# Performance work log

Hardware: AMD Instinct MI355X
Metric: run time of the kernel (lower is better)

The kernel has to match this reference:

```python
import jax, jax.numpy as jnp
import numpy as np

N1 = 128      # neurons_1
N2 = 128      # neurons_2
K = 8         # num_cluster
G = 1000      # number of graphs
NPG = 500     # nodes per graph
N = G * NPG   # total nodes
NEG_SLOPE = 0.45


def setup_inputs() -> dict:
    key = jax.random.key(0)
    ks = jax.random.split(key, 5)
    x = jax.random.normal(ks[0], (N, N1), dtype=jnp.float32)
    cls = jax.random.randint(ks[1], (N,), 0, K, dtype=jnp.int32)
    batch = jnp.repeat(jnp.arange(G, dtype=jnp.int32), NPG)  # sorted graph ids
    W1 = jax.random.normal(ks[2], (N1, N2), dtype=jnp.float32) * 0.05
    b1 = jnp.zeros((N2,), dtype=jnp.float32)
    Wa = jax.random.normal(ks[3], (N2, 1), dtype=jnp.float32) * 0.05
    ba = jnp.zeros((1,), dtype=jnp.float32)
    return {"x": x, "W1": W1, "b1": b1, "Wa": Wa, "ba": ba, "cls": cls, "batch": batch}


def reference(x, W1, b1, Wa, ba, cls, batch):
    # ---- unpooling_featurizer, cluster_method='fixed' (GI-M2), vectorized ----
    # composite segment id: one segment per (graph, cluster)
    seg = batch.astype(jnp.int32) * K + cls.astype(jnp.int32)          # [N]
    csum = jax.ops.segment_sum(x, seg, num_segments=G * K)             # [G*K, N1]
    counts = jax.ops.segment_sum(jnp.ones((N,), jnp.float32), seg,
                                 num_segments=G * K)                   # [G*K]
    # fixed: random_sets == cls, so gather each node's own cluster sum.
    # ratio_i = counts[cls_i]/Ng, renormalized over graph -> counts[cls_i]/sum_k counts_k^2
    cnode = counts[seg]                                                # [N]
    denom = jax.ops.segment_sum(cnode, batch, num_segments=G)          # [G] = sum_k c_k^2
    ratio = cnode / denom[batch]                                       # [N]
    r_x = csum[seg] * ratio[:, None]                                   # [N, N1]
    # ---- attention MLP ----
    h = jax.nn.leaky_relu(r_x @ W1 + b1, negative_slope=NEG_SLOPE)     # [N, N2]
    logits = (h @ Wa + ba)[:, 0]                                       # [N]
    # ---- segment softmax over graphs ----
    m = jax.ops.segment_max(logits, batch, num_segments=G)             # [G]
    z = jnp.exp(logits - m[batch])
    s = jax.ops.segment_sum(z, batch, num_segments=G)
    return (z / s[batch])[:, None]                                     # [N, 1]
```

## Files before the change

kernel.cpp:

```cpp
#include <hip/hip_runtime.h>

#define GG 1000
#define NPG 500
#define KK 8
#define N1 128
#define N2 128
#define NEG_SLOPE 0.45f
#define NTHREADS 512
#define NWAVES 8

__global__ __launch_bounds__(NTHREADS) void cluster_attn_kernel(
    const float* __restrict__ x,
    const float* __restrict__ W1,
    const float* __restrict__ b1,
    const float* __restrict__ Wa,
    const float* __restrict__ ba,
    const int*   __restrict__ cls,
    float*       __restrict__ out)
{
    __shared__ float s_acc[NWAVES][KK][N1];
    __shared__ float s_cnt[NWAVES][KK];
    __shared__ float s_fcnt[KK];
    __shared__ float s_ratio[KK];
    __shared__ float s_L[KK];
    __shared__ float s_e[KK];

    const int g   = blockIdx.x;
    const int tid = threadIdx.x;
    const int w   = tid >> 6;
    const int l   = tid & 63;

    float* accf = &s_acc[0][0][0];

    for (int i = tid; i < NWAVES * KK * N1; i += NTHREADS) accf[i] = 0.f;
    if (tid < NWAVES * KK) s_cnt[tid >> 3][tid & 7] = 0.f;
    __syncthreads();

    const float2* x2   = (const float2*)(x + (size_t)g * NPG * N1);
    const int*    clsg = cls + (size_t)g * NPG;
    float2* accw = (float2*)&s_acc[w][0][0];

    for (int n = w; n < NPG; n += NWAVES) {
        int c = clsg[n];
        float2 v = x2[(size_t)n * 64 + l];
        float2* p = accw + c * 64 + l;
        float2 cur = *p;
        cur.x += v.x; cur.y += v.y;
        *p = cur;
        if (l == 0) s_cnt[w][c] += 1.f;
    }
    __syncthreads();

    for (int e = tid; e < KK * N1; e += NTHREADS) {
        float s = 0.f;
        #pragma unroll
        for (int ww = 0; ww < NWAVES; ++ww) s += s_acc[ww][0][e];
        accf[e] = s;
    }
    if (tid == 0) {
        float d = 0.f;
        #pragma unroll
        for (int k = 0; k < KK; ++k) {
            float c = 0.f;
            #pragma unroll
            for (int ww = 0; ww < NWAVES; ++ww) c += s_cnt[ww][k];
            s_fcnt[k] = c;
            d += c * c;
        }
        #pragma unroll
        for (int k = 0; k < KK; ++k) s_ratio[k] = s_fcnt[k] / d;
    }
    __syncthreads();

    float* s_hw = &s_acc[1][0][0];
    #pragma unroll
    for (int r = 0; r < 2; ++r) {
        int idx = tid + r * NTHREADS;
        int k = idx >> 7;
        int j = idx & 127;
        float s = 0.f;
        #pragma unroll 4
        for (int f = 0; f < N1; ++f)
            s = fmaf(accf[k * N1 + f], W1[f * N2 + j], s);
        float val = fmaf(s, s_ratio[k], b1[j]);
        float h = val > 0.f ? val : NEG_SLOPE * val;
        s_hw[idx] = h * Wa[j];
    }
    __syncthreads();

    {
        float v = s_hw[w * 128 + l] + s_hw[w * 128 + 64 + l];
        #pragma unroll
        for (int off = 32; off > 0; off >>= 1) v += __shfl_down(v, off);
        if (l == 0) s_L[w] = v + ba[0];
    }
    __syncthreads();

    if (tid == 0) {
        float m = -1e30f;
        #pragma unroll
        for (int k = 0; k < KK; ++k)
            if (s_fcnt[k] > 0.f) m = fmaxf(m, s_L[k]);
        float ssum = 0.f;
        float ek[KK];
        #pragma unroll
        for (int k = 0; k < KK; ++k) {
            ek[k] = (s_fcnt[k] > 0.f) ? expf(s_L[k] - m) : 0.f;
            ssum += s_fcnt[k] * ek[k];
        }
        #pragma unroll
        for (int k = 0; k < KK; ++k) s_e[k] = ek[k] / ssum;
    }
    __syncthreads();

    float* outg = out + (size_t)g * NPG;
    for (int n = tid; n < NPG; n += NTHREADS) outg[n] = s_e[clsg[n]];
}

extern "C" void kernel_launch(void* const* d_in, const int* in_sizes, int n_in,
                              void* d_out, int out_size, void* d_ws, size_t ws_size,
                              hipStream_t stream) {
    const float* x   = (const float*)d_in[0];
    const float* W1  = (const float*)d_in[1];
    const float* b1  = (const float*)d_in[2];
    const float* Wa  = (const float*)d_in[3];
    const float* ba  = (const float*)d_in[4];
    const int*   cls = (const int*)d_in[5];

    float* out = (float*)d_out;
    cluster_attn_kernel<<<GG, NTHREADS, 0, stream>>>(x, W1, b1, Wa, ba, cls, out);
}
```

Baseline: 61.29 us.

## Accumulate per-cluster sums in registers with masked FMAs and float4 loads

Replaces the per-wave shared-memory read-modify-write accumulation of each node's cluster sum with register accumulators for all 8 clusters. Each half-wave loads a full node row as float4 and adds it into every cluster slot through a 0/1 mask. Half-waves are combined with a shuffle before the partials are written to shared memory once. Cluster counts now come from shared integer atomics instead of per-wave float counters. This trades 8x redundant FMAs and extra register pressure for fewer LDS round trips, wider loads, and no zero-init pass over shared memory.

```diff
diff --git a/kernel.cpp b/kernel.cpp
--- a/kernel.cpp
+++ b/kernel.cpp
@@ -19,38 +19,62 @@
     float*       __restrict__ out)
 {
     __shared__ float s_acc[NWAVES][KK][N1];
-    __shared__ float s_cnt[NWAVES][KK];
+    __shared__ int   s_icnt[KK];
     __shared__ float s_fcnt[KK];
     __shared__ float s_ratio[KK];
     __shared__ float s_L[KK];
     __shared__ float s_e[KK];
 
-    const int g   = blockIdx.x;
-    const int tid = threadIdx.x;
-    const int w   = tid >> 6;
-    const int l   = tid & 63;
+    const int g    = blockIdx.x;
+    const int tid  = threadIdx.x;
+    const int w    = tid >> 6;
+    const int l    = tid & 63;
+    const int half = l >> 5;
+    const int fs   = l & 31;
 
-    float* accf = &s_acc[0][0][0];
+    const int* clsg = cls + (size_t)g * NPG;
 
-    for (int i = tid; i < NWAVES * KK * N1; i += NTHREADS) accf[i] = 0.f;
-    if (tid < NWAVES * KK) s_cnt[tid >> 3][tid & 7] = 0.f;
+    if (tid < KK) s_icnt[tid] = 0;
     __syncthreads();
+    if (tid < NPG) atomicAdd(&s_icnt[clsg[tid]], 1);
 
-    const float2* x2   = (const float2*)(x + (size_t)g * NPG * N1);
-    const int*    clsg = cls + (size_t)g * NPG;
-    float2* accw = (float2*)&s_acc[w][0][0];
+    float acc[KK][4];
+    #pragma unroll
+    for (int k = 0; k < KK; ++k) {
+        acc[k][0] = 0.f; acc[k][1] = 0.f; acc[k][2] = 0.f; acc[k][3] = 0.f;
+    }
 
-    for (int n = w; n < NPG; n += NWAVES) {
-        int c = clsg[n];
-        float2 v = x2[(size_t)n * 64 + l];
-        float2* p = accw + c * 64 + l;
-        float2 cur = *p;
-        cur.x += v.x; cur.y += v.y;
-        *p = cur;
-        if (l == 0) s_cnt[w][c] += 1.f;
+    const float4* x4 = (const float4*)(x + (size_t)g * NPG * N1);
+    for (int n = w * 2; n < NPG; n += 2 * NWAVES) {
+        int node = n + half;
+        int c = clsg[node];
+        float4 v = x4[(size_t)node * 32 + fs];
+        #pragma unroll
+        for (int k = 0; k < KK; ++k) {
+            float m = (c == k) ? 1.f : 0.f;
+            acc[k][0] = fmaf(m, v.x, acc[k][0]);
+            acc[k][1] = fmaf(m, v.y, acc[k][1]);
+            acc[k][2] = fmaf(m, v.z, acc[k][2]);
+            acc[k][3] = fmaf(m, v.w, acc[k][3]);
+        }
+    }
+
+    #pragma unroll
+    for (int k = 0; k < KK; ++k) {
+        #pragma unroll
+        for (int j = 0; j < 4; ++j)
+            acc[k][j] += __shfl_xor(acc[k][j], 32);
+    }
+    if (l < 32) {
+        #pragma unroll
+        for (int k = 0; k < KK; ++k) {
+            float4* dst = (float4*)&s_acc[w][k][0];
+            dst[fs] = make_float4(acc[k][0], acc[k][1], acc[k][2], acc[k][3]);
+        }
     }
     __syncthreads();
 
+    float* accf = &s_acc[0][0][0];
     for (int e = tid; e < KK * N1; e += NTHREADS) {
         float s = 0.f;
         #pragma unroll
@@ -61,9 +85,7 @@
         float d = 0.f;
         #pragma unroll
         for (int k = 0; k < KK; ++k) {
-            float c = 0.f;
-            #pragma unroll
-            for (int ww = 0; ww < NWAVES; ++ww) c += s_cnt[ww][k];
+            float c = (float)s_icnt[k];
             s_fcnt[k] = c;
             d += c * c;
         }
```

Measured after the change: 71.28 us. 1.16x slower.

## Accumulate cluster sums in registers with wave-uniform switch and unrolled loads

Applied to the files above, without the earlier changes.

Cluster ids for the graph are staged in shared memory, and each wave accumulates its per-cluster partial sums in registers. A wave-uniform switch (readfirstlane) selects the register, replacing the LDS read-modify-write on every node. The node loop is unrolled by four so four row loads are in flight at once. This trades extra registers and a separate shared buffer for fewer LDS round-trips and more memory-level parallelism in the bandwidth-bound streaming phase.

```diff
diff --git a/kernel.cpp b/kernel.cpp
--- a/kernel.cpp
+++ b/kernel.cpp
@@ -19,6 +19,8 @@
     float*       __restrict__ out)
 {
     __shared__ float s_acc[NWAVES][KK][N1];
+    __shared__ float s_hw[KK * N2];
+    __shared__ int   s_cls[NPG];
     __shared__ float s_cnt[NWAVES][KK];
     __shared__ float s_fcnt[KK];
     __shared__ float s_ratio[KK];
@@ -30,27 +32,60 @@
     const int w   = tid >> 6;
     const int l   = tid & 63;
 
-    float* accf = &s_acc[0][0][0];
-
-    for (int i = tid; i < NWAVES * KK * N1; i += NTHREADS) accf[i] = 0.f;
-    if (tid < NWAVES * KK) s_cnt[tid >> 3][tid & 7] = 0.f;
+    const int* clsg = cls + (size_t)g * NPG;
+    if (tid < NPG) s_cls[tid] = clsg[tid];
     __syncthreads();
 
-    const float2* x2   = (const float2*)(x + (size_t)g * NPG * N1);
-    const int*    clsg = cls + (size_t)g * NPG;
-    float2* accw = (float2*)&s_acc[w][0][0];
+    float ax[KK], ay[KK];
+    int   cnt[KK];
+    #pragma unroll
+    for (int k = 0; k < KK; ++k) { ax[k] = 0.f; ay[k] = 0.f; cnt[k] = 0; }
 
-    for (int n = w; n < NPG; n += NWAVES) {
-        int c = clsg[n];
+    const float2* x2 = (const float2*)(x + (size_t)g * NPG * N1);
+
+#define ACCUM(c, v)                                                     \
+    switch (c) {                                                        \
+    case 0: ax[0]+=v.x; ay[0]+=v.y; cnt[0]++; break;                    \
+    case 1: ax[1]+=v.x; ay[1]+=v.y; cnt[1]++; break;                    \
+    case 2: ax[2]+=v.x; ay[2]+=v.y; cnt[2]++; break;                    \
+    case 3: ax[3]+=v.x; ay[3]+=v.y; cnt[3]++; break;                    \
+    case 4: ax[4]+=v.x; ay[4]+=v.y; cnt[4]++; break;                    \
+    case 5: ax[5]+=v.x; ay[5]+=v.y; cnt[5]++; break;                    \
+    case 6: ax[6]+=v.x; ay[6]+=v.y; cnt[6]++; break;                    \
+    default: ax[7]+=v.x; ay[7]+=v.y; cnt[7]++; break;                   \
+    }
+
+    int n = w;
+    for (; n + 3 * NWAVES < NPG; n += 4 * NWAVES) {
+        int c0 = __builtin_amdgcn_readfirstlane(s_cls[n]);
+        int c1 = __builtin_amdgcn_readfirstlane(s_cls[n + NWAVES]);
+        int c2 = __builtin_amdgcn_readfirstlane(s_cls[n + 2 * NWAVES]);
+        int c3 = __builtin_amdgcn_readfirstlane(s_cls[n + 3 * NWAVES]);
+        float2 v0 = x2[(size_t)n * 64 + l];
+        float2 v1 = x2[(size_t)(n + NWAVES) * 64 + l];
+        float2 v2 = x2[(size_t)(n + 2 * NWAVES) * 64 + l];
+        float2 v3 = x2[(size_t)(n + 3 * NWAVES) * 64 + l];
+        ACCUM(c0, v0); ACCUM(c1, v1); ACCUM(c2, v2); ACCUM(c3, v3);
+    }
+    for (; n < NPG; n += NWAVES) {
+        int c = __builtin_amdgcn_readfirstlane(s_cls[n]);
         float2 v = x2[(size_t)n * 64 + l];
-        float2* p = accw + c * 64 + l;
-        float2 cur = *p;
-        cur.x += v.x; cur.y += v.y;
-        *p = cur;
-        if (l == 0) s_cnt[w][c] += 1.f;
+        ACCUM(c, v);
+    }
+#undef ACCUM
+
+    #pragma unroll
+    for (int k = 0; k < KK; ++k) {
+        float2* dst = (float2*)&s_acc[w][k][0];
+        dst[l] = make_float2(ax[k], ay[k]);
+    }
+    if (l == 0) {
+        #pragma unroll
+        for (int k = 0; k < KK; ++k) s_cnt[w][k] = (float)cnt[k];
     }
     __syncthreads();
 
+    float* accf = &s_acc[0][0][0];
     for (int e = tid; e < KK * N1; e += NTHREADS) {
         float s = 0.f;
         #pragma unroll
@@ -72,7 +107,6 @@
     }
     __syncthreads();
 
-    float* s_hw = &s_acc[1][0][0];
     #pragma unroll
     for (int r = 0; r < 2; ++r) {
         int idx = tid + r * NTHREADS;
@@ -114,7 +148,7 @@
     __syncthreads();
 
     float* outg = out + (size_t)g * NPG;
-    for (int n = tid; n < NPG; n += NTHREADS) outg[n] = s_e[clsg[n]];
+    for (int n2 = tid; n2 < NPG; n2 += NTHREADS) outg[n2] = s_e[s_cls[n2]];
 }
 
 extern "C" void kernel_launch(void* const* d_in, const int* in_sizes, int n_in,
```

After: 79.22 us. 1.29x slower.
